# Kernel optimization log

Hardware: AMD Instinct MI355X
Metric: run time of the kernel (lower is better)

The kernel has to match this reference:

```python
import jax, jax.numpy as jnp
import numpy as np

H, C = 4, 64          # heads, head_dim; H*C == hidden_channels == 256
HID = H * C
NT, NC = 50000, 10000
E_TT, E_CT = 400000, 200000
FT, FC = 128, 64


def _gat(xs, xd, att_s, att_d, bias, src, dst, num_dst):
    """PyG GATConv message passing. xs/xd: projected feats [Ns,H,C]/[Nd,H,C]."""
    a = (xs * att_s).sum(-1)[src] + (xd * att_d).sum(-1)[dst]      # [E,H]
    a = jax.nn.leaky_relu(a, 0.2)
    m = jax.ops.segment_max(a, dst, num_segments=num_dst)          # [Nd,H]
    m = jnp.where(jnp.isfinite(m), m, 0.0)
    ex = jnp.exp(a - m[dst])                                       # [E,H]
    den = jax.ops.segment_sum(ex, dst, num_segments=num_dst)       # [Nd,H]
    msg = jax.ops.segment_sum(ex[:, :, None] * xs[src], dst, num_segments=num_dst)  # [Nd,H,C]
    out = msg / jnp.maximum(den, 1e-16)[:, :, None]
    return out.reshape(num_dst, HID) + bias


def setup_inputs() -> dict:
    key = jax.random.key(0)
    ks = jax.random.split(key, 24)

    def glorot(k, shape):
        fan_in = shape[0] if len(shape) > 1 else shape[-1]
        return jax.random.normal(k, shape, jnp.float32) / np.sqrt(fan_in)

    inp = {
        'x_target': jax.random.normal(ks[0], (NT, FT), jnp.float32),
        'x_context': jax.random.normal(ks[1], (NC, FC), jnp.float32),
        'ei_tt': jax.random.randint(ks[2], (2, E_TT), 0, NT, jnp.int32),
        'ei_ct_src': jax.random.randint(ks[3], (E_CT,), 0, NC, jnp.int32),
        'ei_ct_dst': jax.random.randint(ks[4], (E_CT,), 0, NT, jnp.int32),
        # HeteroDictLinear pretransform
        'Wt': glorot(ks[5], (FT, HID)), 'bt': jnp.zeros((HID,), jnp.float32),
        'Wc': glorot(ks[6], (FC, HID)), 'bc': jnp.zeros((HID,), jnp.float32),
        # DirGATConv: src->dst GATConv
        'W_s2d': glorot(ks[7], (HID, HID)),
        'as_s2d': glorot(ks[8], (H, C)), 'ad_s2d': glorot(ks[9], (H, C)),
        'b_s2d': jnp.zeros((HID,), jnp.float32),
        # DirGATConv: dst->src GATConv
        'W_d2s': glorot(ks[10], (HID, HID)),
        'as_d2s': glorot(ks[11], (H, C)), 'ad_d2s': glorot(ks[12], (H, C)),
        'b_d2s': jnp.zeros((HID,), jnp.float32),
        # bipartite context->target GATConv
        'W_ct_src': glorot(ks[13], (HID, HID)), 'W_ct_dst': glorot(ks[14], (HID, HID)),
        'as_ct': glorot(ks[15], (H, C)), 'ad_ct': glorot(ks[16], (H, C)),
        'b_ct': jnp.zeros((HID,), jnp.float32),
        # final Linear(hidden, hidden)
        'W_out': glorot(ks[17], (HID, HID)), 'b_out': jnp.zeros((HID,), jnp.float32),
    }
    return inp


def reference(x_target, x_context, ei_tt, ei_ct_src, ei_ct_dst,
              Wt, bt, Wc, bc,
              W_s2d, as_s2d, ad_s2d, b_s2d,
              W_d2s, as_d2s, ad_d2s, b_d2s,
              W_ct_src, W_ct_dst, as_ct, ad_ct, b_ct,
              W_out, b_out):
    nt = x_target.shape[0]
    # HeteroDictLinear pretransform + relu
    ht = jax.nn.relu(x_target @ Wt + bt)      # [NT, HID]
    hc = jax.nn.relu(x_context @ Wc + bc)     # [NC, HID]

    # homogeneous target-target edges with self-loops (PyG GATConv default)
    loops = jnp.arange(nt, dtype=ei_tt.dtype)
    src = jnp.concatenate([ei_tt[0], loops])
    dst = jnp.concatenate([ei_tt[1], loops])

    # DirGATConv: (1-alpha)*conv(x, ei) + alpha*conv(x, ei^T), alpha=0.5
    p1 = (ht @ W_s2d).reshape(nt, H, C)
    out_s2d = _gat(p1, p1, as_s2d, ad_s2d, b_s2d, src, dst, nt)
    p2 = (ht @ W_d2s).reshape(nt, H, C)
    out_d2s = _gat(p2, p2, as_d2s, ad_d2s, b_d2s, dst, src, nt)
    out_tt = 0.5 * out_s2d + 0.5 * out_d2s

    # bipartite context->target GATConv (no self-loops)
    ps = (hc @ W_ct_src).reshape(hc.shape[0], H, C)
    pd = (ht @ W_ct_dst).reshape(nt, H, C)
    out_ct = _gat(ps, pd, as_ct, ad_ct, b_ct, ei_ct_src, ei_ct_dst, nt)

    # HeteroConv aggr='mean', then skip connection + relu, then final Linear
    x = (out_tt + out_ct) * 0.5
    x = jax.nn.relu(x + ht)
    return x @ W_out + b_out
```

## Files before the change

kernel.cpp:

```cpp
#include <hip/hip_runtime.h>
#include <hip/hip_bf16.h>
#include <cstdint>
#include <cstddef>


#define LRELU_SLOPE 0.2f
#define CAP 64
#define NRANGE 8

typedef __attribute__((ext_vector_type(8))) short short8;
typedef __attribute__((ext_vector_type(4))) float floatx4;

__device__ __forceinline__ float bf2f(ushort u) {
    union { unsigned int u32; float f; } v; v.u32 = ((unsigned int)u) << 16; return v.f;
}
__device__ __forceinline__ ushort f2bf(float x) {
    union { float f; unsigned int u; } v; v.f = x;
    unsigned int r = (v.u + 0x7FFFu + ((v.u >> 16) & 1u)) >> 16;
    return (ushort)r;
}

__global__ __launch_bounds__(256) void prep_all(
    const float* __restrict__ xt, ushort* __restrict__ xtb,
    const float* __restrict__ xc, ushort* __restrict__ xcb,
    const float* __restrict__ Wt,  ushort* __restrict__ WtT,
    const float* __restrict__ Wc,  ushort* __restrict__ WcT,
    const float* __restrict__ W1,  ushort* __restrict__ W1T,
    const float* __restrict__ W2,  ushort* __restrict__ W2T,
    const float* __restrict__ W3,  ushort* __restrict__ W3T,
    const float* __restrict__ W4,  ushort* __restrict__ W4T,
    const float* __restrict__ Wcd, const float* __restrict__ adc,
    float* __restrict__ wfold,
    int s0, int s1, int s2, int s3, int s4, int s5, int s6, int s7, int s8)
{
    const int idx = blockIdx.x * blockDim.x + threadIdx.x;
    if (idx < s0) {
        float4 v = ((const float4*)xt)[idx];
        ushort4 o;
        o.x = f2bf(v.x); o.y = f2bf(v.y); o.z = f2bf(v.z); o.w = f2bf(v.w);
        ((ushort4*)xtb)[idx] = o;
    } else if (idx < s1) {
        const int i = idx - s0;
        float4 v = ((const float4*)xc)[i];
        ushort4 o;
        o.x = f2bf(v.x); o.y = f2bf(v.y); o.z = f2bf(v.z); o.w = f2bf(v.w);
        ((ushort4*)xcb)[i] = o;
    } else if (idx < s2) {
        const int i = idx - s1, k = i >> 8, n = i & 255;
        WtT[n * 128 + k] = f2bf(Wt[i]);
    } else if (idx < s3) {
        const int i = idx - s2, k = i >> 8, n = i & 255;
        WcT[n * 64 + k] = f2bf(Wc[i]);
    } else if (idx < s4) {
        const int i = idx - s3, k = i >> 8, n = i & 255;
        W1T[n * 256 + k] = f2bf(W1[i]);
    } else if (idx < s5) {
        const int i = idx - s4, k = i >> 8, n = i & 255;
        W2T[n * 256 + k] = f2bf(W2[i]);
    } else if (idx < s6) {
        const int i = idx - s5, k = i >> 8, n = i & 255;
        W3T[n * 256 + k] = f2bf(W3[i]);
    } else if (idx < s7) {
        const int i = idx - s6, k = i >> 8, n = i & 255;
        W4T[n * 256 + k] = f2bf(W4[i]);
    } else if (idx < s8) {
        const int i = idx - s7, k = i >> 2, h = i & 3;
        float s = 0.f;
#pragma unroll 8
        for (int c = 0; c < 64; ++c)
            s += Wcd[(size_t)k * 256 + h * 64 + c] * adc[h * 64 + c];
        wfold[i] = s;
    }
}

__device__ __forceinline__ void gemm_core(
    const ushort* __restrict__ A, const ushort* __restrict__ Bt,
    const float* __restrict__ bias, float* __restrict__ Cf,
    ushort* __restrict__ Cb, int M, int K, int do_relu,
    const float* __restrict__ attS, const float* __restrict__ attD,
    float* __restrict__ aSo, float* __restrict__ aDo,
    int row0, int col0)
{
    __shared__ short As[128][40];
    __shared__ short Bs[64][40];
    const int tid  = threadIdx.x;
    const int ra = tid >> 1;
    const int ka = (tid & 1) * 16;
    const int rb = tid >> 2;
    const int kb = (tid & 3) * 8;
    const int w    = tid >> 6;
    const int lane = tid & 63;
    const int cix  = lane & 15;
    const int ksel = (lane >> 4) * 8;

    floatx4 acc[2][4];
#pragma unroll
    for (int r = 0; r < 2; ++r)
#pragma unroll
        for (int c = 0; c < 4; ++c) acc[r][c] = (floatx4){0.f, 0.f, 0.f, 0.f};

    for (int k0 = 0; k0 < K; k0 += 32) {
        short8 a0 = {0,0,0,0,0,0,0,0}, a1 = a0;
        if (row0 + ra < M) {
            const ushort* ap = A + (size_t)(row0 + ra) * K + k0 + ka;
            a0 = *(const short8*)ap;
            a1 = *(const short8*)(ap + 8);
        }
        *(short8*)&As[ra][ka]     = a0;
        *(short8*)&As[ra][ka + 8] = a1;
        *(short8*)&Bs[rb][kb] =
            *(const short8*)(Bt + (size_t)(col0 + rb) * K + k0 + kb);
        __syncthreads();
        const short8 af0 = *(const short8*)&As[32 * w + cix][ksel];
        const short8 af1 = *(const short8*)&As[32 * w + 16 + cix][ksel];
#pragma unroll
        for (int c = 0; c < 4; ++c) {
            const short8 bf = *(const short8*)&Bs[16 * c + cix][ksel];
            acc[0][c] = __builtin_amdgcn_mfma_f32_16x16x32_bf16(af0, bf, acc[0][c], 0, 0, 0);
            acc[1][c] = __builtin_amdgcn_mfma_f32_16x16x32_bf16(af1, bf, acc[1][c], 0, 0, 0);
        }
        __syncthreads();
    }

#pragma unroll
    for (int r = 0; r < 2; ++r) {
        const int rbase = row0 + 32 * w + 16 * r + (lane >> 4) * 4;
#pragma unroll
        for (int c = 0; c < 4; ++c) {
            const int col = col0 + 16 * c + cix;
            const float bv = bias ? bias[col] : 0.f;
#pragma unroll
            for (int i = 0; i < 4; ++i) {
                const int row = rbase + i;
                if (row < M) {
                    float v = acc[r][c][i] + bv;
                    if (do_relu) v = fmaxf(v, 0.f);
                    const size_t off = (size_t)row * 256 + col;
                    if (Cf) Cf[off] = v;
                    if (Cb) Cb[off] = f2bf(v);
                }
            }
        }
    }

    if (attS) {
        float sA[2][4], sD[2][4];
#pragma unroll
        for (int r = 0; r < 2; ++r)
#pragma unroll
            for (int i = 0; i < 4; ++i) { sA[r][i] = 0.f; sD[r][i] = 0.f; }
#pragma unroll
        for (int c = 0; c < 4; ++c) {
            const float as_v = attS[col0 + 16 * c + cix];
            const float ad_v = attD ? attD[col0 + 16 * c + cix] : 0.f;
#pragma unroll
            for (int r = 0; r < 2; ++r)
#pragma unroll
                for (int i = 0; i < 4; ++i) {
                    sA[r][i] += acc[r][c][i] * as_v;
                    sD[r][i] += acc[r][c][i] * ad_v;
                }
        }
#pragma unroll
        for (int off = 1; off < 16; off <<= 1) {
#pragma unroll
            for (int r = 0; r < 2; ++r)
#pragma unroll
                for (int i = 0; i < 4; ++i) {
                    sA[r][i] += __shfl_xor(sA[r][i], off);
                    sD[r][i] += __shfl_xor(sD[r][i], off);
                }
        }
        if (cix == 0) {
            const int head = col0 >> 6;
#pragma unroll
            for (int r = 0; r < 2; ++r) {
                const int rbase = row0 + 32 * w + 16 * r + (lane >> 4) * 4;
#pragma unroll
                for (int i = 0; i < 4; ++i) {
                    const int row = rbase + i;
                    if (row < M) {
                        aSo[(size_t)row * 4 + head] = sA[r][i];
                        if (aDo) aDo[(size_t)row * 4 + head] = sD[r][i];
                    }
                }
            }
        }
    }
}

__global__ __launch_bounds__(256) void gemm_bf16(
    const ushort* __restrict__ A, const ushort* __restrict__ Bt,
    const float* __restrict__ bias, float* __restrict__ Cf,
    ushort* __restrict__ Cb, int M, int K, int do_relu)
{
    const int row0 = blockIdx.x * 128;
    if (row0 >= M) return;
    gemm_core(A, Bt, bias, Cf, Cb, M, K, do_relu,
              nullptr, nullptr, nullptr, nullptr, row0, blockIdx.y * 64);
}

__global__ __launch_bounds__(256) void gemm_pre2(
    const ushort* __restrict__ xtb, const ushort* __restrict__ WtT,
    const float* __restrict__ bt, ushort* __restrict__ htb, int NT,
    const ushort* __restrict__ xcb, const ushort* __restrict__ WcT,
    const float* __restrict__ bc, ushort* __restrict__ hcb, int NC)
{
    const int y = blockIdx.y;
    const int row0 = blockIdx.x * 128;
    if (y < 4) {
        if (row0 >= NT) return;
        gemm_core(xtb, WtT, bt, nullptr, htb, NT, 128, 1,
                  nullptr, nullptr, nullptr, nullptr, row0, y * 64);
    } else {
        if (row0 >= NC) return;
        gemm_core(xcb, WcT, bc, nullptr, hcb, NC, 64, 1,
                  nullptr, nullptr, nullptr, nullptr, row0, (y - 4) * 64);
    }
}

__global__ __launch_bounds__(256) void gemm_proj3(
    const ushort* __restrict__ htb, const ushort* __restrict__ hcb,
    const ushort* __restrict__ W1T, const ushort* __restrict__ W2T,
    const ushort* __restrict__ W3T,
    ushort* __restrict__ Pb1, ushort* __restrict__ Pb2, ushort* __restrict__ PSb,
    const float* __restrict__ as1, const float* __restrict__ ad1,
    const float* __restrict__ as2, const float* __restrict__ ad2,
    const float* __restrict__ asc,
    float* __restrict__ aS1, float* __restrict__ aD1,
    float* __restrict__ aS2, float* __restrict__ aD2,
    float* __restrict__ aSc,
    const float* __restrict__ wfold, float* __restrict__ aDc,
    int NT, int NC)
{
    const int y = blockIdx.y;
    if (y == 12) {
        __shared__ float wf[1024];
        const int tid = threadIdx.x;
        *(float4*)&wf[tid * 4] = *(const float4*)&wfold[tid * 4];
        __syncthreads();
        const int idx = blockIdx.x * 256 + tid;
        if (idx >= NT * 4) return;
        const int n = idx >> 2, h = idx & 3;
        const ushort* row = htb + (size_t)n * 256;
        float s = 0.f;
#pragma unroll
        for (int k = 0; k < 256; k += 4) {
            ushort4 r4 = *(const ushort4*)(row + k);
            s += bf2f(r4.x) * wf[(k + 0) * 4 + h] + bf2f(r4.y) * wf[(k + 1) * 4 + h]
               + bf2f(r4.z) * wf[(k + 2) * 4 + h] + bf2f(r4.w) * wf[(k + 3) * 4 + h];
        }
        aDc[idx] = s;
        return;
    }
    const int row0 = blockIdx.x * 128;
    if (y < 4) {
        if (row0 >= NT) return;
        gemm_core(htb, W1T, nullptr, nullptr, Pb1, NT, 256, 0,
                  as1, ad1, aS1, aD1, row0, y * 64);
    } else if (y < 8) {
        if (row0 >= NT) return;
        gemm_core(htb, W2T, nullptr, nullptr, Pb2, NT, 256, 0,
                  as2, ad2, aS2, aD2, row0, (y - 4) * 64);
    } else {
        if (row0 >= NC) return;
        gemm_core(hcb, W3T, nullptr, nullptr, PSb, NC, 256, 0,
                  asc, nullptr, aSc, nullptr, row0, (y - 8) * 64);
    }
}

__global__ __launch_bounds__(256) void build_all_buckets(
    const int* __restrict__ tt_src, const int* __restrict__ tt_dst, int E_tt,
    const int* __restrict__ ct_src, const int* __restrict__ ct_dst, int E_ct,
    int RS,
    int* __restrict__ cntA, int* __restrict__ bktA,
    int* __restrict__ cntB, int* __restrict__ bktB,
    int* __restrict__ cntC, int* __restrict__ bktC)
{
    const int bx = (blockIdx.x < 512) ? blockIdx.x : blockIdx.x - 512;
    const int range = bx & (NRANGE - 1);
    const int lo = range * RS, hi = lo + RS;
    const int j  = bx >> 3;
    const int stride = 64 * blockDim.x;
    if (blockIdx.x < 512) {
        for (int e = j * blockDim.x + threadIdx.x; e < E_tt; e += stride) {
            const int s = tt_src[e], d = tt_dst[e];
            if (d >= lo && d < hi) {
                const int pa = atomicAdd(&cntA[d], 1);
                if (pa < CAP) bktA[(size_t)d * CAP + pa] = s;
            }
            if (s >= lo && s < hi) {
                const int pb = atomicAdd(&cntB[s], 1);
                if (pb < CAP) bktB[(size_t)s * CAP + pb] = d;
            }
        }
    } else {
        for (int e = j * blockDim.x + threadIdx.x; e < E_ct; e += stride) {
            const int s = ct_src[e], d = ct_dst[e];
            if (d >= lo && d < hi) {
                const int p = atomicAdd(&cntC[d], 1);
                if (p < CAP) bktC[(size_t)d * CAP + p] = s;
            }
        }
    }
}

__device__ __forceinline__ void gat_phase(
    int n, int h, int c4,
    const int* __restrict__ cnt, const int* __restrict__ bkt,
    const float* __restrict__ aS, const float* __restrict__ aD,
    const ushort* __restrict__ X, const float* __restrict__ bias,
    float scale, int has_self, float4& out)
{
    const float aDn = aD[(size_t)n * 4 + h];
    float4 f = {0.f, 0.f, 0.f, 0.f};
    float den = 0.f;
    if (has_self) {
        float a = aS[(size_t)n * 4 + h] + aDn;
        a = (a >= 0.f) ? a : LRELU_SLOPE * a;
        const float w = __expf(a);
        const ushort4 x = *(const ushort4*)(X + (size_t)n * 256 + c4);
        f.x = w * bf2f(x.x); f.y = w * bf2f(x.y);
        f.z = w * bf2f(x.z); f.w = w * bf2f(x.w);
        den = w;
    }
    const int deg = min(cnt[n], CAP);
    const int* b = bkt + (size_t)n * CAP;
    int i = 0;
    for (; i + 4 <= deg; i += 4) {
        const int s0 = b[i], s1 = b[i + 1], s2 = b[i + 2], s3 = b[i + 3];
        float a0 = aS[(size_t)s0 * 4 + h] + aDn;
        float a1 = aS[(size_t)s1 * 4 + h] + aDn;
        float a2 = aS[(size_t)s2 * 4 + h] + aDn;
        float a3 = aS[(size_t)s3 * 4 + h] + aDn;
        a0 = (a0 >= 0.f) ? a0 : LRELU_SLOPE * a0;
        a1 = (a1 >= 0.f) ? a1 : LRELU_SLOPE * a1;
        a2 = (a2 >= 0.f) ? a2 : LRELU_SLOPE * a2;
        a3 = (a3 >= 0.f) ? a3 : LRELU_SLOPE * a3;
        const float w0 = __expf(a0), w1 = __expf(a1);
        const float w2 = __expf(a2), w3 = __expf(a3);
        const ushort4 x0 = *(const ushort4*)(X + (size_t)s0 * 256 + c4);
        const ushort4 x1 = *(const ushort4*)(X + (size_t)s1 * 256 + c4);
        const ushort4 x2 = *(const ushort4*)(X + (size_t)s2 * 256 + c4);
        const ushort4 x3 = *(const ushort4*)(X + (size_t)s3 * 256 + c4);
        f.x += w0 * bf2f(x0.x) + w1 * bf2f(x1.x) + w2 * bf2f(x2.x) + w3 * bf2f(x3.x);
        f.y += w0 * bf2f(x0.y) + w1 * bf2f(x1.y) + w2 * bf2f(x2.y) + w3 * bf2f(x3.y);
        f.z += w0 * bf2f(x0.z) + w1 * bf2f(x1.z) + w2 * bf2f(x2.z) + w3 * bf2f(x3.z);
        f.w += w0 * bf2f(x0.w) + w1 * bf2f(x1.w) + w2 * bf2f(x2.w) + w3 * bf2f(x3.w);
        den += w0 + w1 + w2 + w3;
    }
    for (; i < deg; ++i) {
        const int s = b[i];
        float a = aS[(size_t)s * 4 + h] + aDn;
        a = (a >= 0.f) ? a : LRELU_SLOPE * a;
        const float w = __expf(a);
        const ushort4 x = *(const ushort4*)(X + (size_t)s * 256 + c4);
        f.x += w * bf2f(x.x); f.y += w * bf2f(x.y);
        f.z += w * bf2f(x.z); f.w += w * bf2f(x.w);
        den += w;
    }
    const float inv = 1.f / fmaxf(den, 1e-16f);
    const float4 bv = *(const float4*)(bias + c4);
    out.x += scale * (f.x * inv + bv.x);
    out.y += scale * (f.y * inv + bv.y);
    out.z += scale * (f.z * inv + bv.z);
    out.w += scale * (f.w * inv + bv.w);
}

__global__ __launch_bounds__(256) void gat_gather_fused(
    const int* __restrict__ cntA, const int* __restrict__ bktA,
    const float* __restrict__ aS1, const float* __restrict__ aD1,
    const ushort* __restrict__ P1, const float* __restrict__ b1,
    const int* __restrict__ cntB, const int* __restrict__ bktB,
    const float* __restrict__ aS2, const float* __restrict__ aD2,
    const ushort* __restrict__ P2, const float* __restrict__ b2,
    const int* __restrict__ cntC, const int* __restrict__ bktC,
    const float* __restrict__ aSc, const float* __restrict__ aDc,
    const ushort* __restrict__ Pc, const float* __restrict__ b3,
    ushort* __restrict__ htb, int N)
{
    const int n = blockIdx.x * 4 + (threadIdx.x >> 6);
    if (n >= N) return;
    const int lane = threadIdx.x & 63;
    const int h  = lane >> 4;
    const int c4 = lane << 2;

    float4 out = {0.f, 0.f, 0.f, 0.f};
    gat_phase(n, h, c4, cntA, bktA, aS1, aD1, P1, b1, 0.25f, 1, out);
    gat_phase(n, h, c4, cntB, bktB, aS2, aD2, P2, b2, 0.25f, 1, out);
    gat_phase(n, h, c4, cntC, bktC, aSc, aDc, Pc, b3, 0.50f, 0, out);

    ushort* hp = htb + (size_t)n * 256 + c4;
    const ushort4 hb = *(const ushort4*)hp;
    ushort4 o;
    o.x = f2bf(fmaxf(out.x + bf2f(hb.x), 0.f));
    o.y = f2bf(fmaxf(out.y + bf2f(hb.y), 0.f));
    o.z = f2bf(fmaxf(out.z + bf2f(hb.z), 0.f));
    o.w = f2bf(fmaxf(out.w + bf2f(hb.w), 0.f));
    *(ushort4*)hp = o;
}

extern "C" void kernel_launch(void* const* d_in, const int* in_sizes, int n_in,
                              void* d_out, int out_size, void* d_ws, size_t ws_size,
                              hipStream_t stream)
{
    const int NT   = in_sizes[0] / 128;
    const int NC   = in_sizes[1] / 64;
    const int E_TT = in_sizes[2] / 2;
    const int E_CT = in_sizes[3];

    const float* x_target = (const float*)d_in[0];
    const float* x_context= (const float*)d_in[1];
    const int*   ei_tt    = (const int*)d_in[2];
    const int*   ei_ct_src= (const int*)d_in[3];
    const int*   ei_ct_dst= (const int*)d_in[4];
    const float* Wt   = (const float*)d_in[5];
    const float* bt   = (const float*)d_in[6];
    const float* Wc   = (const float*)d_in[7];
    const float* bc   = (const float*)d_in[8];
    const float* W_s2d  = (const float*)d_in[9];
    const float* as_s2d = (const float*)d_in[10];
    const float* ad_s2d = (const float*)d_in[11];
    const float* b_s2d  = (const float*)d_in[12];
    const float* W_d2s  = (const float*)d_in[13];
    const float* as_d2s = (const float*)d_in[14];
    const float* ad_d2s = (const float*)d_in[15];
    const float* b_d2s  = (const float*)d_in[16];
    const float* W_ct_src = (const float*)d_in[17];
    const float* W_ct_dst = (const float*)d_in[18];
    const float* as_ct  = (const float*)d_in[19];
    const float* ad_ct  = (const float*)d_in[20];
    const float* b_ct   = (const float*)d_in[21];
    const float* W_out  = (const float*)d_in[22];
    const float* b_out  = (const float*)d_in[23];
    float* out = (float*)d_out;

    const int* tt_src = ei_tt;
    const int* tt_dst = ei_tt + E_TT;

    float* ws = (float*)d_ws;
    size_t o = 0;
    ushort* htb = (ushort*)(ws + o);   o += (size_t)NT * 128;
    ushort* Pb1 = (ushort*)(ws + o);   o += (size_t)NT * 128;
    ushort* Pb2 = (ushort*)(ws + o);   o += (size_t)NT * 128;
    ushort* hcb = (ushort*)(ws + o);   o += (size_t)NC * 128;
    ushort* PSb = (ushort*)(ws + o);   o += (size_t)NC * 128;
    ushort* xtb = (ushort*)(ws + o);   o += (size_t)NT * 64;
    ushort* xcb = (ushort*)(ws + o);   o += (size_t)NC * 32;
    int* bktA = (int*)(ws + o);        o += (size_t)NT * CAP;
    int* bktB = (int*)(ws + o);        o += (size_t)NT * CAP;
    int* bktC = (int*)(ws + o);        o += (size_t)NT * CAP;
    float* aS1 = ws + o;               o += (size_t)NT * 4;
    float* aD1 = ws + o;               o += (size_t)NT * 4;
    float* aS2 = ws + o;               o += (size_t)NT * 4;
    float* aD2 = ws + o;               o += (size_t)NT * 4;
    float* aSc = ws + o;               o += (size_t)NT * 4;
    float* aDc = ws + o;               o += (size_t)NT * 4;
    int*   cntA = (int*)(ws + o);      o += (size_t)NT;
    int*   cntB = (int*)(ws + o);      o += (size_t)NT;
    int*   cntC = (int*)(ws + o);      o += (size_t)NT;
    float* wfold = ws + o;             o += 1024;
    ushort* WtT   = (ushort*)(ws + o); o += 128 * 256 / 2;
    ushort* WcT   = (ushort*)(ws + o); o += 64 * 256 / 2;
    ushort* Ws2dT = (ushort*)(ws + o); o += 256 * 256 / 2;
    ushort* Wd2sT = (ushort*)(ws + o); o += 256 * 256 / 2;
    ushort* WctsT = (ushort*)(ws + o); o += 256 * 256 / 2;
    ushort* WoutT = (ushort*)(ws + o); o += 256 * 256 / 2;
    (void)ws_size; (void)n_in; (void)out_size;

    const dim3 blk(256);
    const int gGat = (NT + 3) / 4;
    const int RS = (NT + NRANGE - 1) / NRANGE;
    const int gxT = (NT + 127) / 128;
    const int gxA = (NT * 4 + 255) / 256;

    hipMemsetAsync(cntA, 0, (size_t)NT * 3 * sizeof(int), stream);

    const int s0 = NT * 32;
    const int s1 = s0 + NC * 16;
    const int s2 = s1 + 128 * 256;
    const int s3 = s2 + 64 * 256;
    const int s4 = s3 + 65536;
    const int s5 = s4 + 65536;
    const int s6 = s5 + 65536;
    const int s7 = s6 + 65536;
    const int s8 = s7 + 1024;
    hipLaunchKernelGGL(prep_all, dim3((s8 + 255) / 256), blk, 0, stream,
                       x_target, xtb, x_context, xcb,
                       Wt, WtT, Wc, WcT, W_s2d, Ws2dT, W_d2s, Wd2sT,
                       W_ct_src, WctsT, W_out, WoutT,
                       W_ct_dst, ad_ct, wfold,
                       s0, s1, s2, s3, s4, s5, s6, s7, s8);

    hipLaunchKernelGGL(build_all_buckets, dim3(1024), blk, 0, stream,
                       tt_src, tt_dst, E_TT, ei_ct_src, ei_ct_dst, E_CT, RS,
                       cntA, bktA, cntB, bktB, cntC, bktC);

    hipLaunchKernelGGL(gemm_pre2, dim3(gxT, 8), blk, 0, stream,
                       xtb, WtT, bt, htb, NT, xcb, WcT, bc, hcb, NC);

    hipLaunchKernelGGL(gemm_proj3, dim3(gxA, 13), blk, 0, stream,
                       htb, hcb, Ws2dT, Wd2sT, WctsT, Pb1, Pb2, PSb,
                       as_s2d, ad_s2d, as_d2s, ad_d2s, as_ct,
                       aS1, aD1, aS2, aD2, aSc, wfold, aDc, NT, NC);

    hipLaunchKernelGGL(gat_gather_fused, dim3(gGat), blk, 0, stream,
                       cntA, bktA, aS1, aD1, Pb1, b_s2d,
                       cntB, bktB, aS2, aD2, Pb2, b_d2s,
                       cntC, bktC, aSc, aDc, PSb, b_ct,
                       htb, NT);

    hipLaunchKernelGGL(gemm_bf16, dim3(gxT, 4), blk, 0, stream,
                       htb, WoutT, b_out, out, nullptr, NT, 256, 0);
}
```

Before: 413.0 us.

## Double-buffer GEMM shared-memory tiles to overlap global loads with MFMA

```diff
diff --git a/kernel.cpp b/kernel.cpp
--- a/kernel.cpp
+++ b/kernel.cpp
@@ -81,8 +81,8 @@
     float* __restrict__ aSo, float* __restrict__ aDo,
     int row0, int col0)
 {
-    __shared__ short As[128][40];
-    __shared__ short Bs[64][40];
+    __shared__ short As[2][128][40];
+    __shared__ short Bs[2][64][40];
     const int tid  = threadIdx.x;
     const int ra = tid >> 1;
     const int ka = (tid & 1) * 16;
@@ -92,6 +92,9 @@
     const int lane = tid & 63;
     const int cix  = lane & 15;
     const int ksel = (lane >> 4) * 8;
+    const bool arow_ok = (row0 + ra < M);
+    const ushort* aptr = A + (size_t)(row0 + ra) * K + ka;
+    const ushort* bptr = Bt + (size_t)(col0 + rb) * K + kb;
 
     floatx4 acc[2][4];
 #pragma unroll
@@ -99,27 +102,39 @@
 #pragma unroll
         for (int c = 0; c < 4; ++c) acc[r][c] = (floatx4){0.f, 0.f, 0.f, 0.f};
 
+    short8 sa0 = {0,0,0,0,0,0,0,0}, sa1 = sa0, sb;
+    if (arow_ok) { sa0 = *(const short8*)aptr; sa1 = *(const short8*)(aptr + 8); }
+    sb = *(const short8*)bptr;
+    *(short8*)&As[0][ra][ka]     = sa0;
+    *(short8*)&As[0][ra][ka + 8] = sa1;
+    *(short8*)&Bs[0][rb][kb]     = sb;
+    __syncthreads();
+
+    int cur = 0;
     for (int k0 = 0; k0 < K; k0 += 32) {
-        short8 a0 = {0,0,0,0,0,0,0,0}, a1 = a0;
-        if (row0 + ra < M) {
-            const ushort* ap = A + (size_t)(row0 + ra) * K + k0 + ka;
-            a0 = *(const short8*)ap;
-            a1 = *(const short8*)(ap + 8);
-        }
-        *(short8*)&As[ra][ka]     = a0;
-        *(short8*)&As[ra][ka + 8] = a1;
-        *(short8*)&Bs[rb][kb] =
-            *(const short8*)(Bt + (size_t)(col0 + rb) * K + k0 + kb);
-        __syncthreads();
-        const short8 af0 = *(const short8*)&As[32 * w + cix][ksel];
-        const short8 af1 = *(const short8*)&As[32 * w + 16 + cix][ksel];
+        const bool more = (k0 + 32 < K);
+        if (more) {
+            if (arow_ok) {
+                sa0 = *(const short8*)(aptr + k0 + 32);
+                sa1 = *(const short8*)(aptr + k0 + 40);
+            }
+            sb = *(const short8*)(bptr + k0 + 32);
+        }
+        const short8 af0 = *(const short8*)&As[cur][32 * w + cix][ksel];
+        const short8 af1 = *(const short8*)&As[cur][32 * w + 16 + cix][ksel];
 #pragma unroll
         for (int c = 0; c < 4; ++c) {
-            const short8 bf = *(const short8*)&Bs[16 * c + cix][ksel];
+            const short8 bf = *(const short8*)&Bs[cur][16 * c + cix][ksel];
             acc[0][c] = __builtin_amdgcn_mfma_f32_16x16x32_bf16(af0, bf, acc[0][c], 0, 0, 0);
             acc[1][c] = __builtin_amdgcn_mfma_f32_16x16x32_bf16(af1, bf, acc[1][c], 0, 0, 0);
         }
+        if (more) {
+            *(short8*)&As[cur ^ 1][ra][ka]     = sa0;
+            *(short8*)&As[cur ^ 1][ra][ka + 8] = sa1;
+            *(short8*)&Bs[cur ^ 1][rb][kb]     = sb;
+        }
         __syncthreads();
+        cur ^= 1;
     }
 
 #pragma unroll
```

Result: faster. 404.5 us (-2.0%).
